# Performance work log

Hardware: AMD Instinct MI355X
Metric: run time of the kernel (lower is better)

Reference implementation:

```python
import jax, jax.numpy as jnp
import numpy as np

Q_DIM, KV_DIM, H = 64, 64, 4


def setup_inputs() -> dict:
    key = jax.random.key(0)
    ks = jax.random.split(key, 8)
    b, t = 8, 128
    q_x = jax.random.normal(ks[0], (b, t, Q_DIM), dtype=jnp.float32)
    kv_x = jax.random.normal(ks[1], (b, t, t - 1, KV_DIM), dtype=jnp.float32)
    # nn.Linear weights: (out_features, in_features), applied as x @ W.T
    Wk = jax.random.normal(ks[2], (KV_DIM * H, KV_DIM), dtype=jnp.float32) * 0.05
    Wq = jax.random.normal(ks[3], (KV_DIM * H, Q_DIM), dtype=jnp.float32) * 0.05
    Wv = jax.random.normal(ks[4], (KV_DIM * H, KV_DIM), dtype=jnp.float32) * 0.05
    bias = jax.random.uniform(ks[5], (KV_DIM,), minval=-0.1, maxval=0.1, dtype=jnp.float32)
    Ws = jax.random.normal(ks[6], (1, KV_DIM), dtype=jnp.float32) * 0.05
    bs = jax.random.normal(ks[7], (1,), dtype=jnp.float32) * 0.05
    return {"q_x": q_x, "kv_x": kv_x, "Wk": Wk, "Wq": Wq, "Wv": Wv,
            "bias": bias, "Ws": Ws, "bs": bs}


def reference(q_x, kv_x, Wk, Wq, Wv, bias, Ws, bs):
    b, t, tm1, k = kv_x.shape  # tm1 == t-1
    h = H
    # keys: (b, t, t-1, h, k)
    keys = (kv_x @ Wk.T).reshape(b, t, tm1, h, k)
    # queries: (b, t, 1, h, k)
    queries = (q_x @ Wq.T).reshape(b, t, 1, h, k)
    # additive tanh score projected to scalar per (b,t,n,h)
    act = jnp.tanh(keys + queries + bias)
    score = jnp.einsum('btnhk,k->btnh', act, Ws[0]) + bs[0]
    # softmax over the t-1 key axis (dim=2)
    w = jax.nn.softmax(score, axis=2)  # (b, t, t-1, h)
    values = (kv_x @ Wv.T).reshape(b, t, tm1, h, k)
    # weighted sum over t-1
    x = jnp.einsum('btnh,btnhk->bthk', w, values)
    return x.reshape(b, t, h * k)
```

## Files before the change

### kernel.cpp

```cpp
#include <hip/hip_runtime.h>
#include <math.h>

#define B 8
#define T 128
#define NKEY 127
#define NPAD 128
#define KDIM 64
#define NH 4
#define CH 256

typedef _Float16 half8v __attribute__((ext_vector_type(8)));
typedef float floatx4 __attribute__((ext_vector_type(4)));

__device__ __forceinline__ float fast_tanh(float x) {
    float e = __expf(2.f * x);
    float r = __builtin_amdgcn_rcpf(e + 1.f);
    return fmaf(-2.f, r, 1.f);
}

__device__ __forceinline__ half8v cvt8_rne(const float4& a, const float4& b) {
    half8v h;
    h[0] = (_Float16)a.x; h[1] = (_Float16)a.y;
    h[2] = (_Float16)a.z; h[3] = (_Float16)a.w;
    h[4] = (_Float16)b.x; h[5] = (_Float16)b.y;
    h[6] = (_Float16)b.z; h[7] = (_Float16)b.w;
    return h;
}

__global__ __launch_bounds__(256, 2)
void attn_kernel(const float* __restrict__ q_x,
                 const float* __restrict__ kv_x,
                 const float* __restrict__ Wk,
                 const float* __restrict__ Wq,
                 const float* __restrict__ Wv,
                 const float* __restrict__ bias,
                 const float* __restrict__ Ws,
                 const float* __restrict__ bs,
                 float* __restrict__ out)
{
    __shared__ __align__(16) _Float16 frag[16][64][8];
    __shared__ float qb_lds[CH];
    __shared__ float p_lds[NH][NPAD];
    __shared__ __align__(16) float wkv_lds[NH][KDIM];

    const int bt   = blockIdx.x;
    const int tid  = threadIdx.x;
    const int h    = tid >> 6;
    const int lane = tid & 63;
    const int col  = lane & 15;
    const int quad = lane >> 4;

    const float* __restrict__ kvg = kv_x + (size_t)bt * NKEY * KDIM;

    #pragma unroll
    for (int w = 0; w < 4; ++w) {
        const int chunk = w * 4 + h;
        const int nt = chunk >> 1, ks = chunk & 1;
        const int n  = nt * 16 + (lane & 15);
        const int k0 = ks * 32 + (lane >> 4) * 8;
        float4 a = make_float4(0.f, 0.f, 0.f, 0.f);
        float4 b = make_float4(0.f, 0.f, 0.f, 0.f);
        if (n < NKEY) {
            const float* p = kvg + (size_t)n * KDIM + k0;
            a = *(const float4*)p;
            b = *(const float4*)(p + 4);
        }
        *(half8v*)&frag[chunk][lane][0] = cvt8_rne(a, b);
    }

    {
        const float4* Wq4 = (const float4*)(Wq + (size_t)tid * KDIM);
        const float4* q4g = (const float4*)(q_x + (size_t)bt * KDIM);
        float4 qa = {0.f, 0.f, 0.f, 0.f};
        #pragma unroll
        for (int i = 0; i < 16; ++i) {
            float4 w = Wq4[i];
            float4 q4 = q4g[i];
            qa.x = fmaf(q4.x, w.x, qa.x);
            qa.y = fmaf(q4.y, w.y, qa.y);
            qa.z = fmaf(q4.z, w.z, qa.z);
            qa.w = fmaf(q4.w, w.w, qa.w);
        }
        qb_lds[tid] = (qa.x + qa.y) + (qa.z + qa.w) + bias[tid & 63];
    }

    half8v ah[4][2];
    #pragma unroll
    for (int jt = 0; jt < 4; ++jt)
        #pragma unroll
        for (int ks = 0; ks < 2; ++ks) {
            const float* wrow = Wk + (size_t)(h * 64 + jt * 16 + col) * KDIM
                                   + ks * 32 + quad * 8;
            float4 a = *(const float4*)wrow;
            float4 b = *(const float4*)(wrow + 4);
            ah[jt][ks] = cvt8_rne(a, b);
        }

    __syncthreads();

    float qbv[4][4], wsv[4][4];
    #pragma unroll
    for (int jt = 0; jt < 4; ++jt)
        #pragma unroll
        for (int r = 0; r < 4; ++r) {
            int j = jt * 16 + quad * 4 + r;
            qbv[jt][r] = qb_lds[h * 64 + j];
            wsv[jt][r] = Ws[j];
        }

    #pragma unroll
    for (int nt = 0; nt < 8; ++nt) {
        half8v b0 = *(const half8v*)&frag[nt * 2 + 0][lane][0];
        half8v b1 = *(const half8v*)&frag[nt * 2 + 1][lane][0];

        floatx4 acc[4];
        #pragma unroll
        for (int jt = 0; jt < 4; ++jt) {
            floatx4 c = {0.f, 0.f, 0.f, 0.f};
            c = __builtin_amdgcn_mfma_f32_16x16x32_f16(ah[jt][0], b0, c, 0, 0, 0);
            c = __builtin_amdgcn_mfma_f32_16x16x32_f16(ah[jt][1], b1, c, 0, 0, 0);
            acc[jt] = c;
        }

        float partial = 0.f;
        #pragma unroll
        for (int jt = 0; jt < 4; ++jt)
            #pragma unroll
            for (int r = 0; r < 4; ++r)
                partial = fmaf(fast_tanh(acc[jt][r] + qbv[jt][r]), wsv[jt][r], partial);
        partial += __shfl_xor(partial, 16, 64);
        partial += __shfl_xor(partial, 32, 64);
        if (lane < 16) p_lds[h][nt * 16 + lane] = partial;
    }

    float invl;
    {
        float s_a = p_lds[h][lane];
        float s_b = p_lds[h][64 + lane];
        if (lane == 63) s_b = -1e30f;
        float mx = fmaxf(s_a, s_b);
        #pragma unroll
        for (int off = 32; off > 0; off >>= 1)
            mx = fmaxf(mx, __shfl_xor(mx, off, 64));
        float pa = __expf(s_a - mx);
        float pb = __expf(s_b - mx);
        float ls = pa + pb;
        #pragma unroll
        for (int off = 32; off > 0; off >>= 1)
            ls += __shfl_xor(ls, off, 64);
        invl = 1.f / ls;
        p_lds[h][lane]      = pa;
        p_lds[h][64 + lane] = pb;
    }

    {
        const float* kvl = kvg + lane;
        float w0 = 0.f, w1 = 0.f, w2 = 0.f, w3 = 0.f;
        #pragma unroll 8
        for (int n4 = 0; n4 < NPAD; n4 += 4) {
            float4 p4 = *(const float4*)&p_lds[h][n4];
            const int n3 = (n4 + 3 < NKEY) ? (n4 + 3) : 0;
            w0 = fmaf(p4.x, kvl[(size_t)(n4 + 0) * KDIM], w0);
            w1 = fmaf(p4.y, kvl[(size_t)(n4 + 1) * KDIM], w1);
            w2 = fmaf(p4.z, kvl[(size_t)(n4 + 2) * KDIM], w2);
            w3 = fmaf(p4.w, kvl[(size_t)n3 * KDIM], w3);
        }
        wkv_lds[h][lane] = ((w0 + w1) + (w2 + w3)) * invl;
    }

    {
        const float4* Wv4 = (const float4*)(Wv + (size_t)tid * KDIM);
        const float4* wv_row = (const float4*)wkv_lds[h];
        float4 oa = {0.f, 0.f, 0.f, 0.f};
        #pragma unroll
        for (int i = 0; i < 16; ++i) {
            float4 w = Wv4[i];
            float4 c = wv_row[i];
            oa.x = fmaf(c.x, w.x, oa.x);
            oa.y = fmaf(c.y, w.y, oa.y);
            oa.z = fmaf(c.z, w.z, oa.z);
            oa.w = fmaf(c.w, w.w, oa.w);
        }
        out[(size_t)bt * CH + tid] = (oa.x + oa.y) + (oa.z + oa.w);
    }
}

extern "C" void kernel_launch(void* const* d_in, const int* in_sizes, int n_in,
                              void* d_out, int out_size, void* d_ws, size_t ws_size,
                              hipStream_t stream) {
    const float* q_x  = (const float*)d_in[0];
    const float* kv_x = (const float*)d_in[1];
    const float* Wk   = (const float*)d_in[2];
    const float* Wq   = (const float*)d_in[3];
    const float* Wv   = (const float*)d_in[4];
    const float* bias = (const float*)d_in[5];
    const float* Ws   = (const float*)d_in[6];
    const float* bs   = (const float*)d_in[7];
    float* out = (float*)d_out;

    attn_kernel<<<dim3(B * T), dim3(256), 0, stream>>>(
        q_x, kv_x, Wk, Wq, Wv, bias, Ws, bs, out);
}
```

Measured before the change: 116.5 us.

## Process two query rows per block and prefetch second KV tile during compute

Each block now handles two (b,t) rows instead of one, halving the grid. It loads the Wk fragments and Ws once and computes both query projections together. The second row's KV tile is converted into a second LDS buffer before the first row's compute starts, so its global load latency can overlap that compute. The trade-off is fewer blocks in flight and more LDS per block, which may reduce latency hiding across the GPU.

Result: slower. 124.7 us (+7.0%).

```diff
diff --git a/kernel.cpp b/kernel.cpp
--- a/kernel.cpp
+++ b/kernel.cpp
@@ -25,6 +25,123 @@
     h[4] = (_Float16)b.x; h[5] = (_Float16)b.y;
     h[6] = (_Float16)b.z; h[7] = (_Float16)b.w;
     return h;
+}
+
+__device__ __forceinline__ void stage_kv(_Float16 (*frag)[64][8],
+                                         const float* __restrict__ kvg,
+                                         int h, int lane) {
+    #pragma unroll
+    for (int w = 0; w < 4; ++w) {
+        const int chunk = w * 4 + h;
+        const int nt = chunk >> 1, ks = chunk & 1;
+        const int n  = nt * 16 + (lane & 15);
+        const int k0 = ks * 32 + (lane >> 4) * 8;
+        float4 a = make_float4(0.f, 0.f, 0.f, 0.f);
+        float4 b = make_float4(0.f, 0.f, 0.f, 0.f);
+        if (n < NKEY) {
+            const float* p = kvg + (size_t)n * KDIM + k0;
+            a = *(const float4*)p;
+            b = *(const float4*)(p + 4);
+        }
+        *(half8v*)&frag[chunk][lane][0] = cvt8_rne(a, b);
+    }
+}
+
+__device__ __forceinline__ void compute_bt(
+    const _Float16 (*frag)[64][8],
+    const float* __restrict__ qb,
+    const float* __restrict__ kvg,
+    const float* __restrict__ Wv,
+    float* __restrict__ p_row,
+    float* __restrict__ wkv_row,
+    const float* __restrict__ wkv_base,
+    float* __restrict__ out_bt,
+    const half8v ah[4][2],
+    const float wsv[4][4],
+    int tid, int h, int lane, int quad)
+{
+    float qbv[4][4];
+    #pragma unroll
+    for (int jt = 0; jt < 4; ++jt)
+        #pragma unroll
+        for (int r = 0; r < 4; ++r)
+            qbv[jt][r] = qb[h * 64 + jt * 16 + quad * 4 + r];
+
+    #pragma unroll
+    for (int nt = 0; nt < 8; ++nt) {
+        half8v b0 = *(const half8v*)&frag[nt * 2 + 0][lane][0];
+        half8v b1 = *(const half8v*)&frag[nt * 2 + 1][lane][0];
+
+        floatx4 acc[4];
+        #pragma unroll
+        for (int jt = 0; jt < 4; ++jt) {
+            floatx4 c = {0.f, 0.f, 0.f, 0.f};
+            c = __builtin_amdgcn_mfma_f32_16x16x32_f16(ah[jt][0], b0, c, 0, 0, 0);
+            c = __builtin_amdgcn_mfma_f32_16x16x32_f16(ah[jt][1], b1, c, 0, 0, 0);
+            acc[jt] = c;
+        }
+
+        float partial = 0.f;
+        #pragma unroll
+        for (int jt = 0; jt < 4; ++jt)
+            #pragma unroll
+            for (int r = 0; r < 4; ++r)
+                partial = fmaf(fast_tanh(acc[jt][r] + qbv[jt][r]), wsv[jt][r], partial);
+        partial += __shfl_xor(partial, 16, 64);
+        partial += __shfl_xor(partial, 32, 64);
+        if (lane < 16) p_row[nt * 16 + lane] = partial;
+    }
+
+    float invl;
+    {
+        float s_a = p_row[lane];
+        float s_b = p_row[64 + lane];
+        if (lane == 63) s_b = -1e30f;
+        float mx = fmaxf(s_a, s_b);
+        #pragma unroll
+        for (int off = 32; off > 0; off >>= 1)
+            mx = fmaxf(mx, __shfl_xor(mx, off, 64));
+        float pa = __expf(s_a - mx);
+        float pb = __expf(s_b - mx);
+        float ls = pa + pb;
+        #pragma unroll
+        for (int off = 32; off > 0; off >>= 1)
+            ls += __shfl_xor(ls, off, 64);
+        invl = 1.f / ls;
+        p_row[lane]      = pa;
+        p_row[64 + lane] = pb;
+    }
+
+    {
+        const float* kvl = kvg + lane;
+        float w0 = 0.f, w1 = 0.f, w2 = 0.f, w3 = 0.f;
+        #pragma unroll 8
+        for (int n4 = 0; n4 < NPAD; n4 += 4) {
+            float4 p4 = *(const float4*)&p_row[n4];
+            const int n3 = (n4 + 3 < NKEY) ? (n4 + 3) : 0;
+            w0 = fmaf(p4.x, kvl[(size_t)(n4 + 0) * KDIM], w0);
+            w1 = fmaf(p4.y, kvl[(size_t)(n4 + 1) * KDIM], w1);
+            w2 = fmaf(p4.z, kvl[(size_t)(n4 + 2) * KDIM], w2);
+            w3 = fmaf(p4.w, kvl[(size_t)n3 * KDIM], w3);
+        }
+        wkv_row[lane] = ((w0 + w1) + (w2 + w3)) * invl;
+    }
+
+    {
+        const float4* Wv4 = (const float4*)(Wv + (size_t)tid * KDIM);
+        const float4* wv_row = (const float4*)wkv_base;
+        float4 oa = {0.f, 0.f, 0.f, 0.f};
+        #pragma unroll
+        for (int i = 0; i < 16; ++i) {
+            float4 w = Wv4[i];
+            float4 c = wv_row[i];
+            oa.x = fmaf(c.x, w.x, oa.x);
+            oa.y = fmaf(c.y, w.y, oa.y);
+            oa.z = fmaf(c.z, w.z, oa.z);
+            oa.w = fmaf(c.w, w.w, oa.w);
+        }
+        out_bt[tid] = (oa.x + oa.y) + (oa.z + oa.w);
+    }
 }
 
 __global__ __launch_bounds__(256, 2)
@@ -38,50 +155,46 @@
                  const float* __restrict__ bs,
                  float* __restrict__ out)
 {
-    __shared__ __align__(16) _Float16 frag[16][64][8];
-    __shared__ float qb_lds[CH];
+    __shared__ __align__(16) _Float16 frag[2][16][64][8];
+    __shared__ float qb_lds[2][CH];
     __shared__ float p_lds[NH][NPAD];
     __shared__ __align__(16) float wkv_lds[NH][KDIM];
 
-    const int bt   = blockIdx.x;
+    const int bt0  = blockIdx.x * 2;
     const int tid  = threadIdx.x;
     const int h    = tid >> 6;
     const int lane = tid & 63;
     const int col  = lane & 15;
     const int quad = lane >> 4;
 
-    const float* __restrict__ kvg = kv_x + (size_t)bt * NKEY * KDIM;
-
-    #pragma unroll
-    for (int w = 0; w < 4; ++w) {
-        const int chunk = w * 4 + h;
-        const int nt = chunk >> 1, ks = chunk & 1;
-        const int n  = nt * 16 + (lane & 15);
-        const int k0 = ks * 32 + (lane >> 4) * 8;
-        float4 a = make_float4(0.f, 0.f, 0.f, 0.f);
-        float4 b = make_float4(0.f, 0.f, 0.f, 0.f);
-        if (n < NKEY) {
-            const float* p = kvg + (size_t)n * KDIM + k0;
-            a = *(const float4*)p;
-            b = *(const float4*)(p + 4);
-        }
-        *(half8v*)&frag[chunk][lane][0] = cvt8_rne(a, b);
-    }
+    const float* __restrict__ kvg0 = kv_x + (size_t)bt0 * NKEY * KDIM;
+    const float* __restrict__ kvg1 = kvg0 + (size_t)NKEY * KDIM;
+
+    stage_kv(frag[0], kvg0, h, lane);
 
     {
         const float4* Wq4 = (const float4*)(Wq + (size_t)tid * KDIM);
-        const float4* q4g = (const float4*)(q_x + (size_t)bt * KDIM);
-        float4 qa = {0.f, 0.f, 0.f, 0.f};
+        const float4* q40 = (const float4*)(q_x + (size_t)bt0 * KDIM);
+        const float4* q41 = (const float4*)(q_x + (size_t)(bt0 + 1) * KDIM);
+        float4 a0 = {0.f, 0.f, 0.f, 0.f};
+        float4 a1 = {0.f, 0.f, 0.f, 0.f};
         #pragma unroll
         for (int i = 0; i < 16; ++i) {
-            float4 w = Wq4[i];
-            float4 q4 = q4g[i];
-            qa.x = fmaf(q4.x, w.x, qa.x);
-            qa.y = fmaf(q4.y, w.y, qa.y);
-            qa.z = fmaf(q4.z, w.z, qa.z);
-            qa.w = fmaf(q4.w, w.w, qa.w);
-        }
-        qb_lds[tid] = (qa.x + qa.y) + (qa.z + qa.w) + bias[tid & 63];
+            float4 w  = Wq4[i];
+            float4 qa = q40[i];
+            float4 qc = q41[i];
+            a0.x = fmaf(qa.x, w.x, a0.x);
+            a0.y = fmaf(qa.y, w.y, a0.y);
+            a0.z = fmaf(qa.z, w.z, a0.z);
+            a0.w = fmaf(qa.w, w.w, a0.w);
+            a1.x = fmaf(qc.x, w.x, a1.x);
+            a1.y = fmaf(qc.y, w.y, a1.y);
+            a1.z = fmaf(qc.z, w.z, a1.z);
+            a1.w = fmaf(qc.w, w.w, a1.w);
+        }
+        const float bv = bias[tid & 63];
+        qb_lds[0][tid] = (a0.x + a0.y) + (a0.z + a0.w) + bv;
+        qb_lds[1][tid] = (a1.x + a1.y) + (a1.z + a1.w) + bv;
     }
 
     half8v ah[4][2];
@@ -96,93 +209,28 @@
             ah[jt][ks] = cvt8_rne(a, b);
         }
 
+    float wsv[4][4];
+    #pragma unroll
+    for (int jt = 0; jt < 4; ++jt)
+        #pragma unroll
+        for (int r = 0; r < 4; ++r)
+            wsv[jt][r] = Ws[jt * 16 + quad * 4 + r];
+
     __syncthreads();
 
-    float qbv[4][4], wsv[4][4];
-    #pragma unroll
-    for (int jt = 0; jt < 4; ++jt)
-        #pragma unroll
-        for (int r = 0; r < 4; ++r) {
-            int j = jt * 16 + quad * 4 + r;
-            qbv[jt][r] = qb_lds[h * 64 + j];
-            wsv[jt][r] = Ws[j];
-        }
-
-    #pragma unroll
-    for (int nt = 0; nt < 8; ++nt) {
-        half8v b0 = *(const half8v*)&frag[nt * 2 + 0][lane][0];
-        half8v b1 = *(const half8v*)&frag[nt * 2 + 1][lane][0];
-
-        floatx4 acc[4];
-        #pragma unroll
-        for (int jt = 0; jt < 4; ++jt) {
-            floatx4 c = {0.f, 0.f, 0.f, 0.f};
-            c = __builtin_amdgcn_mfma_f32_16x16x32_f16(ah[jt][0], b0, c, 0, 0, 0);
-            c = __builtin_amdgcn_mfma_f32_16x16x32_f16(ah[jt][1], b1, c, 0, 0, 0);
-            acc[jt] = c;
-        }
-
-        float partial = 0.f;
-        #pragma unroll
-        for (int jt = 0; jt < 4; ++jt)
-            #pragma unroll
-            for (int r = 0; r < 4; ++r)
-                partial = fmaf(fast_tanh(acc[jt][r] + qbv[jt][r]), wsv[jt][r], partial);
-        partial += __shfl_xor(partial, 16, 64);
-        partial += __shfl_xor(partial, 32, 64);
-        if (lane < 16) p_lds[h][nt * 16 + lane] = partial;
-    }
-
-    float invl;
-    {
-        float s_a = p_lds[h][lane];
-        float s_b = p_lds[h][64 + lane];
-        if (lane == 63) s_b = -1e30f;
-        float mx = fmaxf(s_a, s_b);
-        #pragma unroll
-        for (int off = 32; off > 0; off >>= 1)
-            mx = fmaxf(mx, __shfl_xor(mx, off, 64));
-        float pa = __expf(s_a - mx);
-        float pb = __expf(s_b - mx);
-        float ls = pa + pb;
-        #pragma unroll
-        for (int off = 32; off > 0; off >>= 1)
-            ls += __shfl_xor(ls, off, 64);
-        invl = 1.f / ls;
-        p_lds[h][lane]      = pa;
-        p_lds[h][64 + lane] = pb;
-    }
-
-    {
-        const float* kvl = kvg + lane;
-        float w0 = 0.f, w1 = 0.f, w2 = 0.f, w3 = 0.f;
-        #pragma unroll 8
-        for (int n4 = 0; n4 < NPAD; n4 += 4) {
-            float4 p4 = *(const float4*)&p_lds[h][n4];
-            const int n3 = (n4 + 3 < NKEY) ? (n4 + 3) : 0;
-            w0 = fmaf(p4.x, kvl[(size_t)(n4 + 0) * KDIM], w0);
-            w1 = fmaf(p4.y, kvl[(size_t)(n4 + 1) * KDIM], w1);
-            w2 = fmaf(p4.z, kvl[(size_t)(n4 + 2) * KDIM], w2);
-            w3 = fmaf(p4.w, kvl[(size_t)n3 * KDIM], w3);
-        }
-        wkv_lds[h][lane] = ((w0 + w1) + (w2 + w3)) * invl;
-    }
-
-    {
-        const float4* Wv4 = (const float4*)(Wv + (size_t)tid * KDIM);
-        const float4* wv_row = (const float4*)wkv_lds[h];
-        float4 oa = {0.f, 0.f, 0.f, 0.f};
-        #pragma unroll
-        for (int i = 0; i < 16; ++i) {
-            float4 w = Wv4[i];
-            float4 c = wv_row[i];
-            oa.x = fmaf(c.x, w.x, oa.x);
-            oa.y = fmaf(c.y, w.y, oa.y);
-            oa.z = fmaf(c.z, w.z, oa.z);
-            oa.w = fmaf(c.w, w.w, oa.w);
-        }
-        out[(size_t)bt * CH + tid] = (oa.x + oa.y) + (oa.z + oa.w);
-    }
+    stage_kv(frag[1], kvg1, h, lane);
+
+    compute_bt(frag[0], qb_lds[0], kvg0, Wv,
+               p_lds[h], wkv_lds[h], wkv_lds[h],
+               out + (size_t)bt0 * CH,
+               ah, wsv, tid, h, lane, quad);
+
+    __syncthreads();
+
+    compute_bt(frag[1], qb_lds[1], kvg1, Wv,
+               p_lds[h], wkv_lds[h], wkv_lds[h],
+               out + (size_t)(bt0 + 1) * CH,
+               ah, wsv, tid, h, lane, quad);
 }
 
 extern "C" void kernel_launch(void* const* d_in, const int* in_sizes, int n_in,
@@ -198,6 +246,6 @@
     const float* bs   = (const float*)d_in[7];
     float* out = (float*)d_out;
 
-    attn_kernel<<<dim3(B * T), dim3(256), 0, stream>>>(
+    attn_kernel<<<dim3(B * T / 2), dim3(256), 0, stream>>>(
         q_x, kv_x, Wk, Wq, Wv, bias, Ws, bs, out);
 }
```

## Load kv fragments directly from global per head, drop shared staging and block barrier

Applied to the files above, without the earlier changes.

Each wave now loads its own kv_x B-fragments straight from global memory inside the score loop and converts them to fp16 in registers. This replaces the cooperative staging into a shared-memory frag buffer and removes the __syncthreads that separated it from compute. Each of the four head-waves now reads the full kv tile itself, so L2/L1 traffic for kv_x grows by up to four times. Several loops are also unrolled less to cut register pressure. Each wave only reads the qb_lds row it wrote itself, so dropping the barrier stays correct.

Result: slower. 123.7 us (+6.2%).

```diff
diff --git a/kernel.cpp b/kernel.cpp
--- a/kernel.cpp
+++ b/kernel.cpp
@@ -38,8 +38,7 @@
                  const float* __restrict__ bs,
                  float* __restrict__ out)
 {
-    __shared__ __align__(16) _Float16 frag[16][64][8];
-    __shared__ float qb_lds[CH];
+    __shared__ float qb_lds[NH][64];
     __shared__ float p_lds[NH][NPAD];
     __shared__ __align__(16) float wkv_lds[NH][KDIM];
 
@@ -52,27 +51,11 @@
 
     const float* __restrict__ kvg = kv_x + (size_t)bt * NKEY * KDIM;
 
-    #pragma unroll
-    for (int w = 0; w < 4; ++w) {
-        const int chunk = w * 4 + h;
-        const int nt = chunk >> 1, ks = chunk & 1;
-        const int n  = nt * 16 + (lane & 15);
-        const int k0 = ks * 32 + (lane >> 4) * 8;
-        float4 a = make_float4(0.f, 0.f, 0.f, 0.f);
-        float4 b = make_float4(0.f, 0.f, 0.f, 0.f);
-        if (n < NKEY) {
-            const float* p = kvg + (size_t)n * KDIM + k0;
-            a = *(const float4*)p;
-            b = *(const float4*)(p + 4);
-        }
-        *(half8v*)&frag[chunk][lane][0] = cvt8_rne(a, b);
-    }
-
     {
         const float4* Wq4 = (const float4*)(Wq + (size_t)tid * KDIM);
         const float4* q4g = (const float4*)(q_x + (size_t)bt * KDIM);
         float4 qa = {0.f, 0.f, 0.f, 0.f};
-        #pragma unroll
+        #pragma unroll 4
         for (int i = 0; i < 16; ++i) {
             float4 w = Wq4[i];
             float4 q4 = q4g[i];
@@ -81,7 +64,7 @@
             qa.z = fmaf(q4.z, w.z, qa.z);
             qa.w = fmaf(q4.w, w.w, qa.w);
         }
-        qb_lds[tid] = (qa.x + qa.y) + (qa.z + qa.w) + bias[tid & 63];
+        qb_lds[h][lane] = (qa.x + qa.y) + (qa.z + qa.w) + bias[lane];
     }
 
     half8v ah[4][2];
@@ -96,22 +79,30 @@
             ah[jt][ks] = cvt8_rne(a, b);
         }
 
-    __syncthreads();
-
     float qbv[4][4], wsv[4][4];
     #pragma unroll
     for (int jt = 0; jt < 4; ++jt)
         #pragma unroll
         for (int r = 0; r < 4; ++r) {
             int j = jt * 16 + quad * 4 + r;
-            qbv[jt][r] = qb_lds[h * 64 + j];
+            qbv[jt][r] = qb_lds[h][j];
             wsv[jt][r] = Ws[j];
         }
 
-    #pragma unroll
+    #pragma unroll 2
     for (int nt = 0; nt < 8; ++nt) {
-        half8v b0 = *(const half8v*)&frag[nt * 2 + 0][lane][0];
-        half8v b1 = *(const half8v*)&frag[nt * 2 + 1][lane][0];
+        const int n = nt * 16 + col;
+        float4 f0 = {0.f,0.f,0.f,0.f}, f1 = {0.f,0.f,0.f,0.f};
+        float4 f2 = {0.f,0.f,0.f,0.f}, f3 = {0.f,0.f,0.f,0.f};
+        if (n < NKEY) {
+            const float* p = kvg + (size_t)n * KDIM + quad * 8;
+            f0 = *(const float4*)p;
+            f1 = *(const float4*)(p + 4);
+            f2 = *(const float4*)(p + 32);
+            f3 = *(const float4*)(p + 36);
+        }
+        half8v b0 = cvt8_rne(f0, f1);
+        half8v b1 = cvt8_rne(f2, f3);
 
         floatx4 acc[4];
         #pragma unroll
@@ -156,7 +147,7 @@
     {
         const float* kvl = kvg + lane;
         float w0 = 0.f, w1 = 0.f, w2 = 0.f, w3 = 0.f;
-        #pragma unroll 8
+        #pragma unroll 4
         for (int n4 = 0; n4 < NPAD; n4 += 4) {
             float4 p4 = *(const float4*)&p_lds[h][n4];
             const int n3 = (n4 + 3 < NKEY) ? (n4 + 3) : 0;
@@ -172,7 +163,7 @@
         const float4* Wv4 = (const float4*)(Wv + (size_t)tid * KDIM);
         const float4* wv_row = (const float4*)wkv_lds[h];
         float4 oa = {0.f, 0.f, 0.f, 0.f};
-        #pragma unroll
+        #pragma unroll 4
         for (int i = 0; i < 16; ++i) {
             float4 w = Wv4[i];
             float4 c = wv_row[i];
```
